# Optimization experiments

Measured on AMD Instinct MI355X. Metric: run time of the kernel, lower is better.

The kernel has to match this reference:

```python
import jax, jax.numpy as jnp
import numpy as np

D_MODEL, D_FF, H, B, S = 1024, 4096, 16, 4, 2048
D_K = D_MODEL // H
EPS = 1e-5
NEG = -1e9


def _custom_ln(x, alpha, bias):
    # torch: mean, std (unbiased, N-1), alpha*(x-mean)/(std+eps)+bias; alpha/bias scalars
    mean = jnp.mean(x, axis=-1, keepdims=True)
    n = x.shape[-1]
    var = jnp.sum((x - mean) ** 2, axis=-1, keepdims=True) / (n - 1)
    std = jnp.sqrt(var)
    return alpha * (x - mean) / (std + EPS) + bias


def setup_inputs() -> dict:
    key = jax.random.key(0)
    ks = jax.random.split(key, 12)
    sc_d = 1.0 / np.sqrt(D_MODEL)
    sc_f = 1.0 / np.sqrt(D_FF)
    inp = {
        "x": jax.random.normal(ks[0], (B, S, D_MODEL), jnp.float32),
        "src_mask": jnp.ones((B, 1, 1, S), jnp.int32),
        "wq": jax.random.normal(ks[1], (D_MODEL, D_MODEL), jnp.float32) * sc_d,
        "bq": jnp.zeros((D_MODEL,), jnp.float32),
        "wk": jax.random.normal(ks[2], (D_MODEL, D_MODEL), jnp.float32) * sc_d,
        "bk": jnp.zeros((D_MODEL,), jnp.float32),
        "wv": jax.random.normal(ks[3], (D_MODEL, D_MODEL), jnp.float32) * sc_d,
        "bv": jnp.zeros((D_MODEL,), jnp.float32),
        "wo": jax.random.normal(ks[4], (D_MODEL, D_MODEL), jnp.float32) * sc_d,
        "bo": jnp.zeros((D_MODEL,), jnp.float32),
        "w1": jax.random.normal(ks[5], (D_MODEL, D_FF), jnp.float32) * sc_d,
        "b1": jnp.zeros((D_FF,), jnp.float32),
        "w2": jax.random.normal(ks[6], (D_FF, D_MODEL), jnp.float32) * sc_f,
        "b2": jnp.zeros((D_MODEL,), jnp.float32),
        "ln1_a": jnp.ones((1,), jnp.float32),
        "ln1_b": jnp.zeros((1,), jnp.float32),
        "ln2_a": jnp.ones((1,), jnp.float32),
        "ln2_b": jnp.zeros((1,), jnp.float32),
    }
    return inp


def _attention(xn, src_mask, wq, bq, wk, bk, wv, bv, wo, bo):
    q = (xn @ wq + bq).reshape(B, S, H, D_K).transpose(0, 2, 1, 3)  # [B,H,S,Dk]
    k = (xn @ wk + bk).reshape(B, S, H, D_K).transpose(0, 2, 1, 3)
    v = (xn @ wv + bv).reshape(B, S, H, D_K).transpose(0, 2, 1, 3)
    scores = jnp.einsum("bhqd,bhkd->bhqk", q, k) / np.sqrt(D_K)
    scores = jnp.where(src_mask == 0, NEG, scores)
    attn = jax.nn.softmax(scores, axis=-1)
    ctx = jnp.einsum("bhqk,bhkd->bhqd", attn, v)
    ctx = ctx.transpose(0, 2, 1, 3).reshape(B, S, D_MODEL)
    return ctx @ wo + bo


def reference(x, src_mask, wq, bq, wk, bk, wv, bv, wo, bo,
              w1, b1, w2, b2, ln1_a, ln1_b, ln2_a, ln2_b):
    # pre-LN attention residual (dropout=0 -> identity)
    xn = _custom_ln(x, ln1_a, ln1_b)
    x = x + _attention(xn, src_mask, wq, bq, wk, bk, wv, bv, wo, bo)
    # pre-LN FFN residual
    xn = _custom_ln(x, ln2_a, ln2_b)
    ff = jax.nn.relu(xn @ w1 + b1) @ w2 + b2
    return x + ff
```

## Files before the change

kernel.cpp:

```cpp
#include <hip/hip_runtime.h>

typedef unsigned short u16;
typedef __bf16 bf16x8 __attribute__((ext_vector_type(8)));
typedef float f32x4 __attribute__((ext_vector_type(4)));

__device__ __forceinline__ u16 f2bf(float f) {
  unsigned u = __builtin_bit_cast(unsigned, f);
  unsigned lsb = (u >> 16) & 1u;
  u += 0x7fffu + lsb;
  return (u16)(u >> 16);
}

__device__ __forceinline__ unsigned cvt_pk_bf16(float lo, float hi) {
  unsigned r;
  asm("v_cvt_pk_bf16_f32 %0, %1, %2" : "=v"(r) : "v"(lo), "v"(hi));
  return r;
}

__device__ __forceinline__ void gld_lds16(const u16* g, u16* l) {
  __builtin_amdgcn_global_load_lds(
      (__attribute__((address_space(1))) void*)g,
      (__attribute__((address_space(3))) void*)l, 16, 0, 0);
}

__global__ __launch_bounds__(256) void ln_kernel(
    const float* __restrict__ x, u16* __restrict__ out,
    const float* __restrict__ alpha_p, const float* __restrict__ beta_p) {
  const int row = blockIdx.x;
  const int t = threadIdx.x;
  const float4 v = reinterpret_cast<const float4*>(x + (size_t)row * 1024)[t];
  float s = v.x + v.y + v.z + v.w;
  float sq = v.x * v.x + v.y * v.y + v.z * v.z + v.w * v.w;
#pragma unroll
  for (int off = 32; off > 0; off >>= 1) {
    s += __shfl_down(s, off);
    sq += __shfl_down(sq, off);
  }
  __shared__ float red[8];
  const int w = t >> 6;
  if ((t & 63) == 0) { red[w] = s; red[4 + w] = sq; }
  __syncthreads();
  const float ts = red[0] + red[1] + red[2] + red[3];
  const float tq = red[4] + red[5] + red[6] + red[7];
  const float mean = ts * (1.0f / 1024.0f);
  float var = (tq - ts * mean) * (1.0f / 1023.0f);
  var = fmaxf(var, 0.0f);
  const float rden = 1.0f / (sqrtf(var) + 1e-5f);
  const float a = alpha_p[0], bb = beta_p[0];
  uint2 ov;
  ov.x = cvt_pk_bf16(a * (v.x - mean) * rden + bb, a * (v.y - mean) * rden + bb);
  ov.y = cvt_pk_bf16(a * (v.z - mean) * rden + bb, a * (v.w - mean) * rden + bb);
  reinterpret_cast<uint2*>(out + (size_t)row * 1024)[t] = ov;
}

__global__ __launch_bounds__(256) void wcvt_t(
    const float* __restrict__ w, u16* __restrict__ wt, int K, int N, float scale) {
  __shared__ float tile[32][33];
  const int n0 = blockIdx.x * 32, k0 = blockIdx.y * 32;
  const int tx = threadIdx.x, ty = threadIdx.y;
#pragma unroll
  for (int i = 0; i < 4; ++i)
    tile[ty + i * 8][tx] = w[(size_t)(k0 + ty + i * 8) * N + n0 + tx];
  __syncthreads();
#pragma unroll
  for (int i = 0; i < 4; ++i)
    wt[(size_t)(n0 + ty + i * 8) * K + k0 + tx] = f2bf(tile[tx][ty + i * 8] * scale);
}

__global__ __launch_bounds__(256) void pack_bias(
    const float* __restrict__ a, const float* __restrict__ b,
    const float* __restrict__ c, float* __restrict__ o, float qscale) {
  const int i = blockIdx.x * 256 + threadIdx.x;
  o[i] = (i < 1024) ? a[i] * qscale : ((i < 2048) ? b[i - 1024] : c[i - 2048]);
}

__global__ __launch_bounds__(256) void mk_mbias(
    const int* __restrict__ mask, float* __restrict__ mb, int* __restrict__ flags) {
  const int b = blockIdx.x, t = threadIdx.x;
  __shared__ int bad;
  if (t == 0) bad = 0;
  __syncthreads();
  int loc = 0;
#pragma unroll
  for (int i = 0; i < 8; ++i) {
    const int idx = b * 2048 + t * 8 + i;
    const int mv = mask[idx];
    mb[idx] = mv ? 0.f : -1.4427e9f;
    loc |= (mv == 0);
  }
  if (loc) atomicOr(&bad, 1);
  __syncthreads();
  if (t == 0) flags[b] = !bad;
}

template <int EPI, int BM>
__global__ __launch_bounds__(256) void gemm_bt(
    const u16* __restrict__ A, const u16* __restrict__ Bt,
    const float* __restrict__ bias, const float* __restrict__ res,
    void* __restrict__ Cout, u16* __restrict__ vt, int M, int N, int K) {
  constexpr int MF = BM / 32;
  __shared__ u16 As[2][BM * 32];
  __shared__ u16 Bs[2][128 * 32];
  const int tid = threadIdx.x;
  const int l = tid & 63;
  const int w = tid >> 6;
  const int wr = w >> 1, wc = w & 1;
  const int gx = gridDim.x;
  int id = blockIdx.y * gx + blockIdx.x;
  const int nwg = gx * gridDim.y;
  id = (id & 7) * (nwg >> 3) + (id >> 3);
  const int n0 = (id % gx) * 128;
  const int m0 = (id / gx) * BM;
  const int lr = l & 15, lk = (l >> 4) * 8;

  f32x4 acc[MF][4];
#pragma unroll
  for (int i = 0; i < MF; ++i)
#pragma unroll
    for (int j = 0; j < 4; ++j) acc[i][j] = f32x4{0.f, 0.f, 0.f, 0.f};

  const int srow = tid >> 2;
  const int scol = (tid & 3) * 8;
  const u16* gA0 = A + (size_t)(m0 + srow) * K + scol;
  const u16* gA1 = A + (size_t)(m0 + 64 + srow) * K + scol;
  const u16* gB0 = Bt + (size_t)(n0 + srow) * K + scol;
  const u16* gB1 = Bt + (size_t)(n0 + 64 + srow) * K + scol;

  gld_lds16(gA0, &As[0][tid * 8]);
  if constexpr (BM == 128) gld_lds16(gA1, &As[0][2048 + tid * 8]);
  gld_lds16(gB0, &Bs[0][tid * 8]);
  gld_lds16(gB1, &Bs[0][2048 + tid * 8]);
  asm volatile("s_waitcnt vmcnt(0)" ::: "memory");
  __syncthreads();

  int cur = 0;
  for (int k0 = 0; k0 < K; k0 += 32) {
    if (k0 + 32 < K) {
      const int kn = k0 + 32;
      gld_lds16(gA0 + kn, &As[cur ^ 1][tid * 8]);
      if constexpr (BM == 128) gld_lds16(gA1 + kn, &As[cur ^ 1][2048 + tid * 8]);
      gld_lds16(gB0 + kn, &Bs[cur ^ 1][tid * 8]);
      gld_lds16(gB1 + kn, &Bs[cur ^ 1][2048 + tid * 8]);
    }
    bf16x8 a[MF], b[4];
#pragma unroll
    for (int mf = 0; mf < MF; ++mf)
      a[mf] = *reinterpret_cast<const bf16x8*>(&As[cur][(wr * (BM / 2) + mf * 16 + lr) * 32 + lk]);
#pragma unroll
    for (int nf = 0; nf < 4; ++nf)
      b[nf] = *reinterpret_cast<const bf16x8*>(&Bs[cur][(wc * 64 + nf * 16 + lr) * 32 + lk]);
#pragma unroll
    for (int mf = 0; mf < MF; ++mf)
#pragma unroll
      for (int nf = 0; nf < 4; ++nf)
        acc[mf][nf] = __builtin_amdgcn_mfma_f32_16x16x32_bf16(a[mf], b[nf], acc[mf][nf], 0, 0, 0);
    asm volatile("s_waitcnt vmcnt(0)" ::: "memory");
    __syncthreads();
    cur ^= 1;
  }

  if (EPI == 3 && n0 >= 2048) {
#pragma unroll
    for (int mf = 0; mf < MF; ++mf) {
#pragma unroll
      for (int nf = 0; nf < 4; ++nf) {
        const int col = n0 + wc * 64 + nf * 16 + lr;
        const float bv = bias[col];
        const int row0 = m0 + wr * (BM / 2) + mf * 16 + (l >> 4) * 4;
        const int bb = row0 >> 11, s0 = row0 & 2047;
        const int d = col - 2048;
        uint2 pv;
        pv.x = cvt_pk_bf16(acc[mf][nf][0] + bv, acc[mf][nf][1] + bv);
        pv.y = cvt_pk_bf16(acc[mf][nf][2] + bv, acc[mf][nf][3] + bv);
        *reinterpret_cast<uint2*>(vt + ((size_t)bb * 1024 + d) * 2048 + s0) = pv;
      }
    }
    return;
  }

#pragma unroll
  for (int mf = 0; mf < MF; ++mf) {
#pragma unroll
    for (int nf = 0; nf < 4; ++nf) {
      const int col = n0 + wc * 64 + nf * 16 + lr;
      const float bv = bias[col];
#pragma unroll
      for (int j = 0; j < 4; ++j) {
        const int row = m0 + wr * (BM / 2) + mf * 16 + (l >> 4) * 4 + j;
        const size_t idx = (size_t)row * N + col;
        const float vv = acc[mf][nf][j] + bv;
        if (EPI == 0 || EPI == 3)
          ((u16*)Cout)[idx] = f2bf(vv);
        else if (EPI == 1)
          ((float*)Cout)[idx] = vv + res[idx];
        else
          ((u16*)Cout)[idx] = f2bf(fmaxf(vv, 0.f));
      }
    }
  }
}

__global__ __launch_bounds__(256, 4) void attn_fwd7(
    const u16* __restrict__ qkv, const u16* __restrict__ vt,
    const float* __restrict__ mbias, const int* __restrict__ flags,
    u16* __restrict__ ctx) {
  __shared__ u16 Ks[2][64 * 64];
  __shared__ u16 Vs[2][64 * 64];
  const int tid = threadIdx.x;
  const int l = tid & 63;
  const int w = tid >> 6;
  const int p = blockIdx.y * 16 + blockIdx.x;
  const int idx = p >> 3;
  const int bh = (p & 7) * 8 + (idx >> 4);
  const int qx = idx & 15;
  const int b = bh >> 4, h = bh & 15;
  const int r0 = qx * 128 + w * 32;
  const int lr = l & 15, lg = l >> 4;

  const u16* qb = qkv + (size_t)b * 2048 * 3072 + h * 64;
  const u16* kp = qb + 1024;
  const u16* vb = vt + ((size_t)b * 1024 + h * 64) * 2048;
  const float* mb = mbias + (size_t)b * 2048;
  const int allLive = flags[b];

  bf16x8 qf[2][2];
#pragma unroll
  for (int m = 0; m < 2; ++m)
#pragma unroll
    for (int ks = 0; ks < 2; ++ks)
      qf[m][ks] = *reinterpret_cast<const bf16x8*>(
          qb + (size_t)(r0 + m * 16 + lr) * 3072 + ks * 32 + lg * 8);

  bf16x8 ones;
#pragma unroll
  for (int e = 0; e < 8; ++e) ones[e] = (__bf16)1.0f;

  float mrun[2] = {-1e30f, -1e30f};
  f32x4 osum[2];
  f32x4 o[2][4];
#pragma unroll
  for (int m = 0; m < 2; ++m) {
    osum[m] = f32x4{0.f, 0.f, 0.f, 0.f};
#pragma unroll
    for (int d = 0; d < 4; ++d) o[m][d] = f32x4{0.f, 0.f, 0.f, 0.f};
  }

  const u16* kS[2];
  const u16* vS[2];
#pragma unroll
  for (int i = 0; i < 2; ++i) {
    const int ci = tid + i * 256;
    const int row = ci >> 3, cc = ci & 7;
    const int sc = cc ^ (row & 7);
    kS[i] = kp + (size_t)row * 3072 + sc * 8;
    vS[i] = vb + (size_t)row * 2048 + sc * 8;
  }
#pragma unroll
  for (int i = 0; i < 2; ++i) {
    const int ci8 = (tid + i * 256) * 8;
    gld_lds16(kS[i], &Ks[0][ci8]);
    gld_lds16(vS[i], &Vs[0][ci8]);
  }
  asm volatile("s_waitcnt vmcnt(0)" ::: "memory");
  __syncthreads();

  union U8 { unsigned u[4]; bf16x8 v; };

  int cur = 0;
  for (int t = 0; t < 32; ++t) {
    const int kb0 = t * 64;
    if (t + 1 < 32) {
      const int nb = kb0 + 64;
#pragma unroll
      for (int i = 0; i < 2; ++i) {
        const int ci8 = (tid + i * 256) * 8;
        gld_lds16(kS[i] + (size_t)nb * 3072, &Ks[cur ^ 1][ci8]);
        gld_lds16(vS[i] + nb, &Vs[cur ^ 1][ci8]);
      }
    }

    f32x4 st[2][4];
    __builtin_amdgcn_s_setprio(1);
#pragma unroll
    for (int cf = 0; cf < 4; ++cf) {
      const int krow = cf * 16 + lr;
      const int ch0 = lg ^ (krow & 7);
      const int ch1 = (4 + lg) ^ (krow & 7);
      const bf16x8 kf0 = *reinterpret_cast<const bf16x8*>(&Ks[cur][krow * 64 + ch0 * 8]);
      const bf16x8 kf1 = *reinterpret_cast<const bf16x8*>(&Ks[cur][krow * 64 + ch1 * 8]);
#pragma unroll
      for (int m = 0; m < 2; ++m) {
        f32x4 acc = __builtin_amdgcn_mfma_f32_16x16x32_bf16(kf0, qf[m][0],
                                                            f32x4{0.f, 0.f, 0.f, 0.f}, 0, 0, 0);
        st[m][cf] = __builtin_amdgcn_mfma_f32_16x16x32_bf16(kf1, qf[m][1], acc, 0, 0, 0);
      }
    }
    __builtin_amdgcn_s_setprio(0);

    if (!allLive) {
#pragma unroll
      for (int cf = 0; cf < 4; ++cf) {
        const float4 m4 = *reinterpret_cast<const float4*>(mb + kb0 + cf * 16 + lg * 4);
#pragma unroll
        for (int m = 0; m < 2; ++m) {
          st[m][cf][0] += m4.x;
          st[m][cf][1] += m4.y;
          st[m][cf][2] += m4.z;
          st[m][cf][3] += m4.w;
        }
      }
    }

    bf16x8 paA[2], paB[2];
#pragma unroll
    for (int m = 0; m < 2; ++m) {
      float p0 = fmaxf(fmaxf(st[m][0][0], st[m][0][1]), st[m][0][2]);
      float p1 = fmaxf(fmaxf(st[m][0][3], st[m][1][0]), st[m][1][1]);
      float p2 = fmaxf(fmaxf(st[m][1][2], st[m][1][3]), st[m][2][0]);
      float p3 = fmaxf(fmaxf(st[m][2][1], st[m][2][2]), st[m][2][3]);
      float p4 = fmaxf(fmaxf(st[m][3][0], st[m][3][1]), st[m][3][2]);
      float pm = fmaxf(fmaxf(p0, p1), p2);
      pm = fmaxf(fmaxf(pm, p3), p4);
      pm = fmaxf(pm, st[m][3][3]);
      pm = fmaxf(pm, __shfl_xor(pm, 16));
      pm = fmaxf(pm, __shfl_xor(pm, 32));
      if (__any(pm > mrun[m] + 8.f)) {
        const float mn = fmaxf(mrun[m], pm);
        const float corr = exp2f(mrun[m] - mn);
        mrun[m] = mn;
#pragma unroll
        for (int j = 0; j < 4; ++j) osum[m][j] *= corr;
#pragma unroll
        for (int d = 0; d < 4; ++d)
#pragma unroll
          for (int j = 0; j < 4; ++j) o[m][d][j] *= corr;
      }
#pragma unroll
      for (int cf = 0; cf < 4; ++cf)
#pragma unroll
        for (int j = 0; j < 4; ++j)
          st[m][cf][j] = exp2f(st[m][cf][j] - mrun[m]);

      unsigned pk[4][2];
#pragma unroll
      for (int cf = 0; cf < 4; ++cf)
#pragma unroll
        for (int wp = 0; wp < 2; ++wp)
          pk[cf][wp] = cvt_pk_bf16(st[m][cf][2 * wp], st[m][cf][2 * wp + 1]);

      U8 a0, a1;
#pragma unroll
      for (int c = 0; c < 2; ++c) {
        const int src = lr + 16 * ((2 * lg + c) & 3);
#pragma unroll
        for (int wp = 0; wp < 2; ++wp) {
          const int v00 = __shfl((int)pk[0][wp], src);
          const int v01 = __shfl((int)pk[1][wp], src);
          const int v10 = __shfl((int)pk[2][wp], src);
          const int v11 = __shfl((int)pk[3][wp], src);
          a0.u[2 * c + wp] = (unsigned)((lg < 2) ? v00 : v01);
          a1.u[2 * c + wp] = (unsigned)((lg < 2) ? v10 : v11);
        }
      }
      paA[m] = a0.v;
      paB[m] = a1.v;
    }

    __builtin_amdgcn_s_setprio(1);
#pragma unroll
    for (int df = 0; df < 4; ++df) {
      const int vrow = df * 16 + lr;
      const int ch0 = lg ^ (vrow & 7);
      const int ch1 = (4 + lg) ^ (vrow & 7);
      const bf16x8 vf0 = *reinterpret_cast<const bf16x8*>(&Vs[cur][vrow * 64 + ch0 * 8]);
      const bf16x8 vf1 = *reinterpret_cast<const bf16x8*>(&Vs[cur][vrow * 64 + ch1 * 8]);
#pragma unroll
      for (int m = 0; m < 2; ++m) {
        o[m][df] = __builtin_amdgcn_mfma_f32_16x16x32_bf16(vf0, paA[m], o[m][df], 0, 0, 0);
        o[m][df] = __builtin_amdgcn_mfma_f32_16x16x32_bf16(vf1, paB[m], o[m][df], 0, 0, 0);
      }
    }
#pragma unroll
    for (int m = 0; m < 2; ++m) {
      osum[m] = __builtin_amdgcn_mfma_f32_16x16x32_bf16(ones, paA[m], osum[m], 0, 0, 0);
      osum[m] = __builtin_amdgcn_mfma_f32_16x16x32_bf16(ones, paB[m], osum[m], 0, 0, 0);
    }
    __builtin_amdgcn_s_setprio(0);

    asm volatile("s_waitcnt vmcnt(0)" ::: "memory");
    __syncthreads();
    cur ^= 1;
  }

#pragma unroll
  for (int m = 0; m < 2; ++m) {
    const float rdiv = 1.f / osum[m][0];
    const size_t rowbase = ((size_t)b * 2048 + r0 + m * 16 + lr) * 1024 + h * 64;
#pragma unroll
    for (int df = 0; df < 4; ++df) {
      uint2 s4;
      s4.x = cvt_pk_bf16(o[m][df][0] * rdiv, o[m][df][1] * rdiv);
      s4.y = cvt_pk_bf16(o[m][df][2] * rdiv, o[m][df][3] * rdiv);
      *reinterpret_cast<uint2*>(ctx + rowbase + df * 16 + lg * 4) = s4;
    }
  }
}

extern "C" void kernel_launch(void* const* d_in, const int* in_sizes, int n_in,
                              void* d_out, int out_size, void* d_ws, size_t ws_size,
                              hipStream_t stream) {
  const float* x = (const float*)d_in[0];
  const int* mask = (const int*)d_in[1];
  const float* wq = (const float*)d_in[2];
  const float* bq = (const float*)d_in[3];
  const float* wk = (const float*)d_in[4];
  const float* bk = (const float*)d_in[5];
  const float* wv = (const float*)d_in[6];
  const float* bv = (const float*)d_in[7];
  const float* wo = (const float*)d_in[8];
  const float* bo = (const float*)d_in[9];
  const float* w1 = (const float*)d_in[10];
  const float* b1 = (const float*)d_in[11];
  const float* w2 = (const float*)d_in[12];
  const float* b2 = (const float*)d_in[13];
  const float* ln1a = (const float*)d_in[14];
  const float* ln1b = (const float*)d_in[15];
  const float* ln2a = (const float*)d_in[16];
  const float* ln2b = (const float*)d_in[17];

  const float SCL2 = 0.125f * 1.4426950408889634f;

  char* ws = (char*)d_ws;
  const size_t MB = 1024ull * 1024ull;
  u16* WTQKV = (u16*)(ws + 0 * MB);
  u16* WTO = (u16*)(ws + 6 * MB);
  u16* W1T = (u16*)(ws + 8 * MB);
  u16* W2T = (u16*)(ws + 16 * MB);
  float* BQKV = (float*)(ws + 24 * MB);
  float* MBIAS = (float*)(ws + 24 * MB + 65536);
  int* FLAGS = (int*)(ws + 24 * MB + 131072);
  u16* QKV = (u16*)(ws + 25 * MB);
  u16* VT = (u16*)(ws + 73 * MB);
  u16* XN = (u16*)(ws + 89 * MB);
  u16* CTX = (u16*)(ws + 105 * MB);
  float* X2 = (float*)(ws + 25 * MB);
  u16* XN2 = (u16*)(ws + 57 * MB);
  u16* H1 = (u16*)(ws + 73 * MB);

  dim3 bt(32, 8);
  wcvt_t<<<dim3(32, 32), bt, 0, stream>>>(wq, WTQKV, 1024, 1024, SCL2);
  wcvt_t<<<dim3(32, 32), bt, 0, stream>>>(wk, WTQKV + 1024 * 1024, 1024, 1024, 1.f);
  wcvt_t<<<dim3(32, 32), bt, 0, stream>>>(wv, WTQKV + 2048 * 1024, 1024, 1024, 1.f);
  wcvt_t<<<dim3(32, 32), bt, 0, stream>>>(wo, WTO, 1024, 1024, 1.f);
  wcvt_t<<<dim3(128, 32), bt, 0, stream>>>(w1, W1T, 1024, 4096, 1.f);
  wcvt_t<<<dim3(32, 128), bt, 0, stream>>>(w2, W2T, 4096, 1024, 1.f);
  pack_bias<<<dim3(12), 256, 0, stream>>>(bq, bk, bv, BQKV, SCL2);
  mk_mbias<<<dim3(4), 256, 0, stream>>>(mask, MBIAS, FLAGS);

  ln_kernel<<<8192, 256, 0, stream>>>(x, XN, ln1a, ln1b);
  gemm_bt<3, 128><<<dim3(24, 64), 256, 0, stream>>>(XN, WTQKV, BQKV, nullptr, QKV, VT, 8192, 3072, 1024);
  attn_fwd7<<<dim3(16, 64), 256, 0, stream>>>(QKV, VT, MBIAS, FLAGS, CTX);
  gemm_bt<1, 64><<<dim3(8, 128), 256, 0, stream>>>(CTX, WTO, bo, x, X2, nullptr, 8192, 1024, 1024);
  ln_kernel<<<8192, 256, 0, stream>>>(X2, XN2, ln2a, ln2b);
  gemm_bt<2, 128><<<dim3(32, 64), 256, 0, stream>>>(XN2, W1T, b1, nullptr, H1, nullptr, 8192, 4096, 1024);
  gemm_bt<1, 64><<<dim3(8, 128), 256, 0, stream>>>(H1, W2T, b2, X2, (float*)d_out, nullptr, 8192, 1024, 4096);
}
```

Baseline: 486.9 us.

## Rewrite GEMM with 512-thread 256-wide tiles, triple-buffered LDS and swizzle

Replaces the 256-thread double-buffered GEMM with a 512-thread, 8-wave kernel using 256-column tiles (BM 256 or 128). LDS is now dynamic and triple-buffered so that loads for the tile two steps ahead are in flight during compute, and the wait uses partial vmcnt instead of draining everything. An XOR swizzle of the k-chunk offset is meant to avoid LDS bank conflicts, and s_setprio raises wave priority around the MFMA block. Larger tiles improve data reuse but cut the number of workgroups and raise LDS use, which can hurt occupancy and wave-count balance across CUs.

```diff
diff --git a/kernel.cpp b/kernel.cpp
--- a/kernel.cpp
+++ b/kernel.cpp
@@ -94,24 +94,28 @@
 }
 
 template <int EPI, int BM>
-__global__ __launch_bounds__(256) void gemm_bt(
+__global__ __launch_bounds__(512, BM == 256 ? 2 : 4) void gemm8(
     const u16* __restrict__ A, const u16* __restrict__ Bt,
     const float* __restrict__ bias, const float* __restrict__ res,
     void* __restrict__ Cout, u16* __restrict__ vt, int M, int N, int K) {
   constexpr int MF = BM / 32;
-  __shared__ u16 As[2][BM * 32];
-  __shared__ u16 Bs[2][128 * 32];
+  constexpr int NA = (BM == 256) ? 2 : 1;
+  extern __shared__ u16 smem[];
+  u16* Asb = smem;
+  u16* Bsb = smem + 3 * BM * 32;
+
   const int tid = threadIdx.x;
   const int l = tid & 63;
   const int w = tid >> 6;
-  const int wr = w >> 1, wc = w & 1;
+  const int wr = w >> 2, wc = w & 3;
   const int gx = gridDim.x;
   int id = blockIdx.y * gx + blockIdx.x;
   const int nwg = gx * gridDim.y;
   id = (id & 7) * (nwg >> 3) + (id >> 3);
-  const int n0 = (id % gx) * 128;
+  const int n0 = (id % gx) * 256;
   const int m0 = (id / gx) * BM;
-  const int lr = l & 15, lk = (l >> 4) * 8;
+  const int lr = l & 15, lg = l >> 4;
+  const int koff = (lg ^ ((lr >> 1) & 3)) * 8;
 
   f32x4 acc[MF][4];
 #pragma unroll
@@ -119,44 +123,74 @@
 #pragma unroll
     for (int j = 0; j < 4; ++j) acc[i][j] = f32x4{0.f, 0.f, 0.f, 0.f};
 
-  const int srow = tid >> 2;
-  const int scol = (tid & 3) * 8;
-  const u16* gA0 = A + (size_t)(m0 + srow) * K + scol;
-  const u16* gA1 = A + (size_t)(m0 + 64 + srow) * K + scol;
-  const u16* gB0 = Bt + (size_t)(n0 + srow) * K + scol;
-  const u16* gB1 = Bt + (size_t)(n0 + 64 + srow) * K + scol;
-
-  gld_lds16(gA0, &As[0][tid * 8]);
-  if constexpr (BM == 128) gld_lds16(gA1, &As[0][2048 + tid * 8]);
-  gld_lds16(gB0, &Bs[0][tid * 8]);
-  gld_lds16(gB1, &Bs[0][2048 + tid * 8]);
-  asm volatile("s_waitcnt vmcnt(0)" ::: "memory");
-  __syncthreads();
+  const u16* aSrc[NA];
+  int aOff[NA];
+#pragma unroll
+  for (int i = 0; i < NA; ++i) {
+    const int ci = tid + i * 512;
+    const int row = ci >> 2, c = ci & 3;
+    const int sc = c ^ ((row >> 1) & 3);
+    aSrc[i] = A + (size_t)(m0 + row) * K + sc * 8;
+    aOff[i] = ci * 8;
+  }
+  const u16* bSrc[2];
+  int bOff[2];
+#pragma unroll
+  for (int i = 0; i < 2; ++i) {
+    const int ci = tid + i * 512;
+    const int row = ci >> 2, c = ci & 3;
+    const int sc = c ^ ((row >> 1) & 3);
+    bSrc[i] = Bt + (size_t)(n0 + row) * K + sc * 8;
+    bOff[i] = ci * 8;
+  }
+
+  const int NT = K >> 5;
+#pragma unroll
+  for (int i = 0; i < NA; ++i) gld_lds16(aSrc[i], Asb + aOff[i]);
+#pragma unroll
+  for (int i = 0; i < 2; ++i) gld_lds16(bSrc[i], Bsb + bOff[i]);
+#pragma unroll
+  for (int i = 0; i < NA; ++i) gld_lds16(aSrc[i] + 32, Asb + BM * 32 + aOff[i]);
+#pragma unroll
+  for (int i = 0; i < 2; ++i) gld_lds16(bSrc[i] + 32, Bsb + 256 * 32 + bOff[i]);
+  if constexpr (NA == 2) asm volatile("s_waitcnt vmcnt(4)" ::: "memory");
+  else asm volatile("s_waitcnt vmcnt(3)" ::: "memory");
+  __builtin_amdgcn_s_barrier();
 
   int cur = 0;
-  for (int k0 = 0; k0 < K; k0 += 32) {
-    if (k0 + 32 < K) {
-      const int kn = k0 + 32;
-      gld_lds16(gA0 + kn, &As[cur ^ 1][tid * 8]);
-      if constexpr (BM == 128) gld_lds16(gA1 + kn, &As[cur ^ 1][2048 + tid * 8]);
-      gld_lds16(gB0 + kn, &Bs[cur ^ 1][tid * 8]);
-      gld_lds16(gB1 + kn, &Bs[cur ^ 1][2048 + tid * 8]);
-    }
+  for (int t = 0; t < NT; ++t) {
+    const int nx2 = (cur + 2 >= 3) ? cur - 1 : cur + 2;
+    if (t + 2 < NT) {
+      const int ko = (t + 2) * 32;
+#pragma unroll
+      for (int i = 0; i < NA; ++i) gld_lds16(aSrc[i] + ko, Asb + nx2 * BM * 32 + aOff[i]);
+#pragma unroll
+      for (int i = 0; i < 2; ++i) gld_lds16(bSrc[i] + ko, Bsb + nx2 * 256 * 32 + bOff[i]);
+    }
+    const u16* Ab = Asb + cur * BM * 32;
+    const u16* Bb = Bsb + cur * 256 * 32;
     bf16x8 a[MF], b[4];
 #pragma unroll
     for (int mf = 0; mf < MF; ++mf)
-      a[mf] = *reinterpret_cast<const bf16x8*>(&As[cur][(wr * (BM / 2) + mf * 16 + lr) * 32 + lk]);
+      a[mf] = *reinterpret_cast<const bf16x8*>(&Ab[(wr * (BM / 2) + mf * 16 + lr) * 32 + koff]);
 #pragma unroll
     for (int nf = 0; nf < 4; ++nf)
-      b[nf] = *reinterpret_cast<const bf16x8*>(&Bs[cur][(wc * 64 + nf * 16 + lr) * 32 + lk]);
+      b[nf] = *reinterpret_cast<const bf16x8*>(&Bb[(wc * 64 + nf * 16 + lr) * 32 + koff]);
+    __builtin_amdgcn_s_setprio(1);
 #pragma unroll
     for (int mf = 0; mf < MF; ++mf)
 #pragma unroll
       for (int nf = 0; nf < 4; ++nf)
         acc[mf][nf] = __builtin_amdgcn_mfma_f32_16x16x32_bf16(a[mf], b[nf], acc[mf][nf], 0, 0, 0);
-    asm volatile("s_waitcnt vmcnt(0)" ::: "memory");
-    __syncthreads();
-    cur ^= 1;
+    __builtin_amdgcn_s_setprio(0);
+    if (t + 2 < NT) {
+      if constexpr (NA == 2) asm volatile("s_waitcnt vmcnt(4)" ::: "memory");
+      else asm volatile("s_waitcnt vmcnt(3)" ::: "memory");
+    } else {
+      asm volatile("s_waitcnt vmcnt(0)" ::: "memory");
+    }
+    __builtin_amdgcn_s_barrier();
+    cur = (cur + 1 >= 3) ? 0 : cur + 1;
   }
 
   if (EPI == 3 && n0 >= 2048) {
@@ -166,7 +200,7 @@
       for (int nf = 0; nf < 4; ++nf) {
         const int col = n0 + wc * 64 + nf * 16 + lr;
         const float bv = bias[col];
-        const int row0 = m0 + wr * (BM / 2) + mf * 16 + (l >> 4) * 4;
+        const int row0 = m0 + wr * (BM / 2) + mf * 16 + lg * 4;
         const int bb = row0 >> 11, s0 = row0 & 2047;
         const int d = col - 2048;
         uint2 pv;
@@ -186,15 +220,15 @@
       const float bv = bias[col];
 #pragma unroll
       for (int j = 0; j < 4; ++j) {
-        const int row = m0 + wr * (BM / 2) + mf * 16 + (l >> 4) * 4 + j;
+        const int row = m0 + wr * (BM / 2) + mf * 16 + lg * 4 + j;
         const size_t idx = (size_t)row * N + col;
         const float vv = acc[mf][nf][j] + bv;
-        if (EPI == 0 || EPI == 3)
+        if (EPI == 1)
+          ((float*)Cout)[idx] = vv + res[idx];
+        else if (EPI == 2)
+          ((u16*)Cout)[idx] = f2bf(fmaxf(vv, 0.f));
+        else
           ((u16*)Cout)[idx] = f2bf(vv);
-        else if (EPI == 1)
-          ((float*)Cout)[idx] = vv + res[idx];
-        else
-          ((u16*)Cout)[idx] = f2bf(fmaxf(vv, 0.f));
       }
     }
   }
@@ -429,6 +463,15 @@
   const float* ln2b = (const float*)d_in[17];
 
   const float SCL2 = 0.125f * 1.4426950408889634f;
+  const size_t LDS256 = 3 * (256 + 256) * 32 * sizeof(u16);
+  const size_t LDS128 = 3 * (128 + 256) * 32 * sizeof(u16);
+
+  hipFuncSetAttribute((const void*)&gemm8<3, 256>,
+                      hipFuncAttributeMaxDynamicSharedMemorySize, (int)LDS256);
+  hipFuncSetAttribute((const void*)&gemm8<2, 256>,
+                      hipFuncAttributeMaxDynamicSharedMemorySize, (int)LDS256);
+  hipFuncSetAttribute((const void*)&gemm8<1, 128>,
+                      hipFuncAttributeMaxDynamicSharedMemorySize, (int)LDS128);
 
   char* ws = (char*)d_ws;
   const size_t MB = 1024ull * 1024ull;
@@ -458,10 +501,10 @@
   mk_mbias<<<dim3(4), 256, 0, stream>>>(mask, MBIAS, FLAGS);
 
   ln_kernel<<<8192, 256, 0, stream>>>(x, XN, ln1a, ln1b);
-  gemm_bt<3, 128><<<dim3(24, 64), 256, 0, stream>>>(XN, WTQKV, BQKV, nullptr, QKV, VT, 8192, 3072, 1024);
+  gemm8<3, 256><<<dim3(12, 32), 512, LDS256, stream>>>(XN, WTQKV, BQKV, nullptr, QKV, VT, 8192, 3072, 1024);
   attn_fwd7<<<dim3(16, 64), 256, 0, stream>>>(QKV, VT, MBIAS, FLAGS, CTX);
-  gemm_bt<1, 64><<<dim3(8, 128), 256, 0, stream>>>(CTX, WTO, bo, x, X2, nullptr, 8192, 1024, 1024);
+  gemm8<1, 128><<<dim3(4, 64), 512, LDS128, stream>>>(CTX, WTO, bo, x, X2, nullptr, 8192, 1024, 1024);
   ln_kernel<<<8192, 256, 0, stream>>>(X2, XN2, ln2a, ln2b);
-  gemm_bt<2, 128><<<dim3(32, 64), 256, 0, stream>>>(XN2, W1T, b1, nullptr, H1, nullptr, 8192, 4096, 1024);
-  gemm_bt<1, 64><<<dim3(8, 128), 256, 0, stream>>>(H1, W2T, b2, X2, (float*)d_out, nullptr, 8192, 1024, 4096);
-}
+  gemm8<2, 256><<<dim3(16, 32), 512, LDS256, stream>>>(XN2, W1T, b1, nullptr, H1, nullptr, 8192, 4096, 1024);
+  gemm8<1, 128><<<dim3(4, 64), 512, LDS128, stream>>>(H1, W2T, b2, X2, (float*)d_out, nullptr, 8192, 1024, 4096);
+}
```

Result: faster. 455.4 us (-6.5%).
